# Performance work log

Measured on AMD Instinct MI355X. Metric: run time of the kernel, lower is better.

The kernel has to match this reference:

```python
import jax, jax.numpy as jnp
import numpy as np

B, L, H, K = 16, 65536, 64, 64


def setup_inputs() -> dict:
    key = jax.random.key(0)
    k1, k2 = jax.random.split(key, 2)
    x = jax.random.normal(k1, (B, L), dtype=jnp.float32)
    W = jax.random.normal(k2, (K, H), dtype=jnp.float32) * 0.02  # nn.Linear weight [K, H]
    b = jnp.zeros((K,), dtype=jnp.float32)
    return {"x": x, "W": W, "b": b}


def reference(x, W, b):
    # x: [B, L]; W: [K, H]; b: [K]
    Hh = W.shape[1]
    Bb, Ll = x.shape
    xpad = jnp.pad(x, ((0, 0), (Hh - 1, 0)))  # left-pad like F.pad(x, (H-1, 0))
    # Hankel windows: windows[b, t, j] = xpad[b, t + j]  -> [B, L, H]
    idx = jnp.arange(Ll)[:, None] + jnp.arange(Hh)[None, :]
    windows = xpad[:, idx]
    mu = windows.mean(axis=2, keepdims=True)
    sd = windows.std(axis=2, keepdims=True, ddof=1)  # torch std is unbiased (ddof=1)
    wn = (windows - mu) / (sd + 1e-6)
    d2 = jax.nn.relu(jnp.einsum('blh,kh->blk', wn, W) + b)
    warmup = Hh - 1
    return (d2[:, warmup:, :], warmup)
```

## Files before the change

kernel.cpp:

```cpp
#include <hip/hip_runtime.h>
#include <hip/hip_bf16.h>
#include <stdint.h>

#define LCOUNT 65536
#define LOUT   65473
#define KF     64
#define HH     64
#define TL     1024

typedef __attribute__((ext_vector_type(8))) short  short8;
typedef __attribute__((ext_vector_type(4))) float  float4v;

__device__ __forceinline__ unsigned short f2bf(float f) {
    union { float f; uint32_t u; } c; c.f = f;
    uint32_t u = c.u;
    u += 0x7FFFu + ((u >> 16) & 1u);
    return (unsigned short)(u >> 16);
}

__global__ __launch_bounds__(256)
void hankel_kernel(const float* __restrict__ x,
                   const float* __restrict__ W,
                   const float* __restrict__ bias,
                   float* __restrict__ out)
{
    __shared__ float          xs_f[TL + 64];
    __shared__ unsigned short xs_b[TL + 64];
    __shared__ float          mu_s[TL];
    __shared__ float          inv_s[TL];
    __shared__ float          wsum_s[KF];
    __shared__ float          bias_s[KF];

    const int tid  = threadIdx.x;
    const int lane = tid & 63;
    const int wv   = tid >> 6;
    const int m    = lane & 15;
    const int quad = lane >> 4;

    const int tile     = blockIdx.x;
    const int bb       = blockIdx.y;
    const int block_lo = tile * TL;

    {
        const float4v* xrow4 = (const float4v*)(x + (size_t)bb * LCOUNT);
        const int base4 = block_lo >> 2;
        const int nf4   = (TL + 64) / 4;
        for (int i4 = tid; i4 < nf4; i4 += 256) {
            int g4 = base4 + i4;
            if (g4 > LCOUNT / 4 - 1) g4 = LCOUNT / 4 - 1;
            float4v v = xrow4[g4];
            *(float4v*)(xs_f + 4 * i4) = v;
            uint32_t plo = (uint32_t)f2bf(v[0]) | ((uint32_t)f2bf(v[1]) << 16);
            uint32_t phi = (uint32_t)f2bf(v[2]) | ((uint32_t)f2bf(v[3]) << 16);
            uint2* dst = (uint2*)(xs_b + 4 * i4);
            *dst = make_uint2(plo, phi);
        }
    }

    if (tid < KF) {
        const float4v* wr = (const float4v*)(W + tid * HH);
        float s = 0.f;
        #pragma unroll
        for (int i = 0; i < HH / 4; ++i) {
            float4v w = wr[i];
            s += w[0] + w[1] + w[2] + w[3];
        }
        wsum_s[tid] = s;
        bias_s[tid] = bias[tid];
    }

    short8 afrag[4][2];
    #pragma unroll
    for (int t = 0; t < 4; ++t) {
        const int k = t * 16 + m;
        #pragma unroll
        for (int ki = 0; ki < 2; ++ki) {
            const float4v* wp = (const float4v*)(W + k * HH + quad * 8 + ki * 32);
            float4v w0 = wp[0];
            float4v w1 = wp[1];
            short8 f;
            f[0] = (short)f2bf(w0[0]); f[1] = (short)f2bf(w0[1]);
            f[2] = (short)f2bf(w0[2]); f[3] = (short)f2bf(w0[3]);
            f[4] = (short)f2bf(w1[0]); f[5] = (short)f2bf(w1[1]);
            f[6] = (short)f2bf(w1[2]); f[7] = (short)f2bf(w1[3]);
            afrag[t][ki] = f;
        }
    }

    __syncthreads();

    {
        const int p0 = 4 * tid;
        const float4v* xv = (const float4v*)(xs_f + p0);
        float s1 = 0.f, s2 = 0.f;
        float4v v0 = xv[0];
        float4v v16 = xv[16];
        #pragma unroll
        for (int i = 0; i < 16; ++i) {
            float4v v = xv[i];
            s1 += v[0] + v[1] + v[2] + v[3];
            s2 += v[0] * v[0] + v[1] * v[1] + v[2] * v[2] + v[3] * v[3];
        }
        float4v muv, invv;
        #pragma unroll
        for (int i = 0; i < 4; ++i) {
            if (i > 0) {
                float xo = v0[i - 1], xn = v16[i - 1];
                s1 += xn - xo;
                s2 += xn * xn - xo * xo;
            }
            float mu  = s1 * (1.f / 64.f);
            float var = (s2 - 64.f * mu * mu) * (1.f / 63.f);
            var = var < 0.f ? 0.f : var;
            muv[i]  = mu;
            invv[i] = 1.f / (sqrtf(var) + 1e-6f);
        }
        *(float4v*)(mu_s + p0)  = muv;
        *(float4v*)(inv_s + p0) = invv;
    }
    __syncthreads();

    for (int g = wv; g < TL / 16; g += 4) {
        const int p0    = g * 16;
        const int abase = p0 + m + quad * 8;

        short8 b0, b1;
        #pragma unroll
        for (int j = 0; j < 8; ++j) {
            b0[j] = (short)xs_b[abase + j];
            b1[j] = (short)xs_b[abase + 32 + j];
        }

        const float muv  = mu_s[p0 + m];
        const float invv = inv_s[p0 + m];
        const int   lo   = block_lo + p0 + m;

        float4v acc[4];
        #pragma unroll
        for (int t = 0; t < 4; ++t) acc[t] = (float4v){0.f, 0.f, 0.f, 0.f};

        #pragma unroll
        for (int t = 0; t < 4; ++t) {
            acc[t] = __builtin_amdgcn_mfma_f32_16x16x32_bf16(afrag[t][0], b0, acc[t], 0, 0, 0);
            acc[t] = __builtin_amdgcn_mfma_f32_16x16x32_bf16(afrag[t][1], b1, acc[t], 0, 0, 0);
        }

        if (lo < LOUT) {
            float* op = out + ((size_t)bb * LOUT + lo) * KF + quad * 4;
            #pragma unroll
            for (int t = 0; t < 4; ++t) {
                float4v ws = *(const float4v*)(wsum_s + t * 16 + quad * 4);
                float4v bs = *(const float4v*)(bias_s + t * 16 + quad * 4);
                float4v v;
                #pragma unroll
                for (int r = 0; r < 4; ++r) {
                    float vv = (acc[t][r] - muv * ws[r]) * invv + bs[r];
                    v[r] = vv > 0.f ? vv : 0.f;
                }
                *(float4v*)(op + t * 16) = v;
            }
        }
    }

    if (tile == 0 && bb == 0 && tid == 0) {
        out[(size_t)16 * LOUT * KF] = 63.0f;
    }
}

extern "C" void kernel_launch(void* const* d_in, const int* in_sizes, int n_in,
                              void* d_out, int out_size, void* d_ws, size_t ws_size,
                              hipStream_t stream) {
    const float* x = (const float*)d_in[0];
    const float* W = (const float*)d_in[1];
    const float* b = (const float*)d_in[2];
    float* out = (float*)d_out;

    dim3 grid((LOUT + TL - 1) / TL, 16);
    hankel_kernel<<<grid, 256, 0, stream>>>(x, W, b, out);
}
```

Measured before the change: 282.3 us.

## Replicate bf16 row into eight shifted copies for vectorized LDS fragment loads

```diff
diff --git a/kernel.cpp b/kernel.cpp
--- a/kernel.cpp
+++ b/kernel.cpp
@@ -7,9 +7,11 @@
 #define KF     64
 #define HH     64
 #define TL     1024
+#define ROW    1096
 
 typedef __attribute__((ext_vector_type(8))) short  short8;
 typedef __attribute__((ext_vector_type(4))) float  float4v;
+typedef __attribute__((ext_vector_type(2))) float  float2v;
 
 __device__ __forceinline__ unsigned short f2bf(float f) {
     union { float f; uint32_t u; } c; c.f = f;
@@ -18,18 +20,17 @@
     return (unsigned short)(u >> 16);
 }
 
-__global__ __launch_bounds__(256)
+__global__ __launch_bounds__(256, 4)
 void hankel_kernel(const float* __restrict__ x,
                    const float* __restrict__ W,
                    const float* __restrict__ bias,
                    float* __restrict__ out)
 {
-    __shared__ float          xs_f[TL + 64];
-    __shared__ unsigned short xs_b[TL + 64];
-    __shared__ float          mu_s[TL];
-    __shared__ float          inv_s[TL];
-    __shared__ float          wsum_s[KF];
-    __shared__ float          bias_s[KF];
+    __shared__ __align__(16) float          xs_f[TL + 64];
+    __shared__ __align__(16) unsigned short rep[8 * ROW];
+    __shared__ __align__(16) float          muinv_s[2 * TL];
+    __shared__ float wsum_s[KF];
+    __shared__ float bias_s[KF];
 
     const int tid  = threadIdx.x;
     const int lane = tid & 63;
@@ -52,8 +53,7 @@
             *(float4v*)(xs_f + 4 * i4) = v;
             uint32_t plo = (uint32_t)f2bf(v[0]) | ((uint32_t)f2bf(v[1]) << 16);
             uint32_t phi = (uint32_t)f2bf(v[2]) | ((uint32_t)f2bf(v[3]) << 16);
-            uint2* dst = (uint2*)(xs_b + 4 * i4);
-            *dst = make_uint2(plo, phi);
+            *(uint2*)(rep + 4 * i4) = make_uint2(plo, phi);
         }
     }
 
@@ -101,7 +101,7 @@
             s1 += v[0] + v[1] + v[2] + v[3];
             s2 += v[0] * v[0] + v[1] * v[1] + v[2] * v[2] + v[3] * v[3];
         }
-        float4v muv, invv;
+        float mu4[4], inv4[4];
         #pragma unroll
         for (int i = 0; i < 4; ++i) {
             if (i > 0) {
@@ -112,27 +112,40 @@
             float mu  = s1 * (1.f / 64.f);
             float var = (s2 - 64.f * mu * mu) * (1.f / 63.f);
             var = var < 0.f ? 0.f : var;
-            muv[i]  = mu;
-            invv[i] = 1.f / (sqrtf(var) + 1e-6f);
+            mu4[i]  = mu;
+            inv4[i] = 1.f / (sqrtf(var) + 1e-6f);
         }
-        *(float4v*)(mu_s + p0)  = muv;
-        *(float4v*)(inv_s + p0) = invv;
+        float4v lo4, hi4;
+        lo4[0] = mu4[0]; lo4[1] = inv4[0]; lo4[2] = mu4[1]; lo4[3] = inv4[1];
+        hi4[0] = mu4[2]; hi4[1] = inv4[2]; hi4[2] = mu4[3]; hi4[3] = inv4[3];
+        *(float4v*)(muinv_s + 8 * tid)     = lo4;
+        *(float4v*)(muinv_s + 8 * tid + 4) = hi4;
+    }
+
+    for (int tt = tid; tt < 1080; tt += 256) {
+        const int s = tt & 7;
+        const int c = tt >> 3;
+        if (s) {
+            const int i0 = 8 * c + s;
+            short8 w;
+            #pragma unroll
+            for (int j = 0; j < 8; ++j) w[j] = (short)rep[i0 + j];
+            *(short8*)(rep + s * ROW + 8 * c) = w;
+        }
     }
     __syncthreads();
 
+    const unsigned short* myrow = rep + (m & 7) * ROW + (m & 8) + quad * 8;
+
     for (int g = wv; g < TL / 16; g += 4) {
-        const int p0    = g * 16;
-        const int abase = p0 + m + quad * 8;
+        const int p0 = g * 16;
 
-        short8 b0, b1;
-        #pragma unroll
-        for (int j = 0; j < 8; ++j) {
-            b0[j] = (short)xs_b[abase + j];
-            b1[j] = (short)xs_b[abase + 32 + j];
-        }
+        short8 b0 = *(const short8*)(myrow + p0);
+        short8 b1 = *(const short8*)(myrow + p0 + 32);
 
-        const float muv  = mu_s[p0 + m];
-        const float invv = inv_s[p0 + m];
+        float2v mi = *(const float2v*)(muinv_s + 2 * (p0 + m));
+        const float muv  = mi[0];
+        const float invv = mi[1];
         const int   lo   = block_lo + p0 + m;
 
         float4v acc[4];
```

Measured after the change: 279.7 us. Within noise of the previous version (-0.9%).
